# Performance work log

Hardware: AMD Instinct MI355X
Metric: run time of the kernel (lower is better)

The kernel has to match this reference:

```python
import jax, jax.numpy as jnp
import numpy as np

B, T, E, H = 4, 4096, 512, 64

def setup_inputs() -> dict:
    key = jax.random.key(0)
    k1, k2, k3, k4 = jax.random.split(key, 4)
    x = jax.random.normal(k1, (B, T, E), dtype=jnp.float32)
    # nn.Linear(E, H, bias=False) weight has shape [H, E]; y = x @ W.T
    Wq = jax.random.normal(k2, (H, E), dtype=jnp.float32) * (E ** -0.5)
    Wk = jax.random.normal(k3, (H, E), dtype=jnp.float32) * (E ** -0.5)
    Wv = jax.random.normal(k4, (H, E), dtype=jnp.float32) * (E ** -0.5)
    return {"x": x, "Wq": Wq, "Wk": Wk, "Wv": Wv}

def reference(x, Wq, Wk, Wv):
    # projections: [B, T, H]
    q = jnp.einsum('bte,he->bth', x, Wq)
    k = jnp.einsum('bte,he->bth', x, Wk)
    v = jnp.einsum('bte,he->bth', x, Wv)
    scale = 1.0 / jnp.sqrt(jnp.float32(q.shape[-1]))
    scores = jnp.einsum('bth,bsh->bts', q, k) * scale  # [B, T, T]
    t = scores.shape[-1]
    causal = jnp.tril(jnp.ones((t, t), dtype=bool))
    scores = jnp.where(causal, scores, -jnp.inf)
    probs = jax.nn.softmax(scores, axis=-1)
    # dropout p=0.0 (eval) -> identity
    return jnp.einsum('bts,bsh->bth', probs, v)
```

## Files before the change

kernel.cpp:

```cpp
#include <hip/hip_runtime.h>
#include <hip/hip_bf16.h>

#define Bn 4
#define Tn 4096
#define En 512
#define Hn 64
#define NEGINF -3e38f
#define QSCALE 0.1803368801f

typedef __attribute__((ext_vector_type(8))) __bf16 bf16x8;
typedef __attribute__((ext_vector_type(4))) __bf16 bf16x4;
typedef __attribute__((ext_vector_type(4))) float f32x4;

#define MFMA16(a, b, c) __builtin_amdgcn_mfma_f32_16x16x32_bf16(a, b, c, 0, 0, 0)

__device__ __forceinline__ unsigned short f2bf(float f) {
    union { float f; unsigned u; } v; v.f = f;
    unsigned r = v.u + 0x7fffu + ((v.u >> 16) & 1u);
    return (unsigned short)(r >> 16);
}
__device__ __forceinline__ float bf2f(unsigned short u) {
    union { unsigned u; float f; } v; v.u = ((unsigned)u) << 16;
    return v.f;
}
__device__ __forceinline__ unsigned cvtpk(float a, float b) {
    unsigned d;
    asm("v_cvt_pk_bf16_f32 %0, %1, %2" : "=v"(d) : "v"(a), "v"(b));
    return d;
}
__device__ __forceinline__ float exp2fast(float x) {
    float r;
    asm("v_exp_f32 %0, %1" : "=v"(r) : "v"(x));
    return r;
}
__device__ __forceinline__ void gl16(const void* g, void* l) {
    __builtin_amdgcn_global_load_lds(
        (const __attribute__((address_space(1))) unsigned int*)g,
        (__attribute__((address_space(3))) unsigned int*)l, 16, 0, 0);
}

__global__ void wcvt(const float* __restrict__ Wq, const float* __restrict__ Wk,
                     const float* __restrict__ Wv, unsigned short* __restrict__ Wo) {
    int i = blockIdx.x * 256 + threadIdx.x;
    int mat = i >> 15;
    int off = i & 32767;
    const float* s = (mat == 0) ? Wq : ((mat == 1) ? Wk : Wv);
    Wo[i] = f2bf(s[off]);
}

__launch_bounds__(256, 2)
__global__ void proj(const float* __restrict__ x, const unsigned short* __restrict__ Wo,
                     unsigned short* __restrict__ q16, unsigned short* __restrict__ k16,
                     unsigned short* __restrict__ vt16) {
    __shared__ __align__(16) unsigned char plds[2][28672];
    const int tid = threadIdx.x;
    const int w = tid >> 6, lane = tid & 63, r = lane & 15, g = lane >> 4;
    const int row0 = blockIdx.x * 32;
    const int rsel = (w & 1) * 16, csel = (w >> 1) * 96;

    const int srow = tid >> 3, skc = (tid & 7) * 8;
    const int sby = (tid & 7) * 16;

    f32x4 acc[6];
#pragma unroll
    for (int i = 0; i < 6; ++i) acc[i] = (f32x4){0.f, 0.f, 0.f, 0.f};

    {
        const float4* xp = (const float4*)&x[(row0 + srow) * En + skc];
        float4 f0 = xp[0], f1 = xp[1];
        union { bf16x8 v; unsigned u32[4]; } t;
        t.u32[0] = cvtpk(f0.x, f0.y); t.u32[1] = cvtpk(f0.z, f0.w);
        t.u32[2] = cvtpk(f1.x, f1.y); t.u32[3] = cvtpk(f1.z, f1.w);
        *(bf16x8*)&plds[0][srow * 128 + (sby ^ ((srow & 7) << 4))] = t.v;
#pragma unroll
        for (int c2 = 0; c2 < 6; ++c2) {
            int wrow = c2 * 32 + srow;
            bf16x8 wv = *(const bf16x8*)&Wo[wrow * En + skc];
            *(bf16x8*)&plds[0][4096 + wrow * 128 + (sby ^ ((wrow & 7) << 4))] = wv;
        }
    }
    __syncthreads();

    for (int s = 0; s < 8; ++s) {
        const int pp = s & 1;
        const bool more = (s < 7);
        float4 nf0, nf1;
        bf16x8 nw[6];
        if (more) {
            int k1 = (s + 1) * 64;
            const float4* xp = (const float4*)&x[(row0 + srow) * En + k1 + skc];
            nf0 = xp[0]; nf1 = xp[1];
#pragma unroll
            for (int c2 = 0; c2 < 6; ++c2) {
                int wrow = c2 * 32 + srow;
                nw[c2] = *(const bf16x8*)&Wo[wrow * En + k1 + skc];
            }
        }
        {
            const unsigned char* A = &plds[pp][0];
            const unsigned char* W = &plds[pp][4096];
            int arow = rsel + r, asw = (arow & 7) << 4;
            bf16x8 a0 = *(const bf16x8*)&A[arow * 128 + ((g * 16) ^ asw)];
            bf16x8 a1 = *(const bf16x8*)&A[arow * 128 + ((64 + g * 16) ^ asw)];
#pragma unroll
            for (int ct = 0; ct < 6; ++ct) {
                int wrow = csel + ct * 16 + r, wsw = (wrow & 7) << 4;
                bf16x8 b0 = *(const bf16x8*)&W[wrow * 128 + ((g * 16) ^ wsw)];
                bf16x8 b1 = *(const bf16x8*)&W[wrow * 128 + ((64 + g * 16) ^ wsw)];
                acc[ct] = MFMA16(a0, b0, acc[ct]);
                acc[ct] = MFMA16(a1, b1, acc[ct]);
            }
        }
        if (more) {
            unsigned char* D = &plds[pp ^ 1][0];
            union { bf16x8 v; unsigned u32[4]; } t;
            t.u32[0] = cvtpk(nf0.x, nf0.y); t.u32[1] = cvtpk(nf0.z, nf0.w);
            t.u32[2] = cvtpk(nf1.x, nf1.y); t.u32[3] = cvtpk(nf1.z, nf1.w);
            *(bf16x8*)&D[srow * 128 + (sby ^ ((srow & 7) << 4))] = t.v;
#pragma unroll
            for (int c2 = 0; c2 < 6; ++c2) {
                int wrow = c2 * 32 + srow;
                *(bf16x8*)&D[4096 + wrow * 128 + (sby ^ ((wrow & 7) << 4))] = nw[c2];
            }
        }
        __syncthreads();
    }
#pragma unroll
    for (int ct = 0; ct < 6; ++ct) {
        int n = csel + ct * 16 + r;
#pragma unroll
        for (int reg = 0; reg < 4; ++reg) {
            int gr = row0 + rsel + g * 4 + reg;
            if (n < 64) {
                q16[gr * 64 + n] = f2bf(acc[ct][reg] * QSCALE);
            } else if (n < 128) {
                k16[gr * 64 + (n - 64)] = f2bf(acc[ct][reg]);
            } else {
                int h = n - 128; int bb = gr >> 12; int t = gr & 4095;
                vt16[((bb * 64 + h) << 12) + t] = f2bf(acc[ct][reg]);
            }
        }
    }
}

__launch_bounds__(256, 4)
__global__ void attnp(const unsigned short* __restrict__ q16, const unsigned short* __restrict__ k16,
                      const unsigned short* __restrict__ vt16,
                      unsigned short* __restrict__ po, float* __restrict__ lp) {
    __shared__ __align__(16) unsigned char lds[2][16384];

    const int tid = threadIdx.x;
    const int w = tid >> 6, lane = tid & 63, r = lane & 15, g = lane >> 4;
    const int bid = blockIdx.x;
    const int k_ = bid >> 8, idx = bid & 255;
    const int s5 = idx >> 3, b = (idx >> 1) & 3, q1 = idx & 1;
    const int jt = (k_ & 1) ? s5 : 63 - s5;
    const int quarter = ((k_ >> 1) << 1) | q1;
    const size_t kbase = (size_t)b * Tn;
    const int q0 = jt * 64;
    const int nt = jt + 1;
    const int t0 = (quarter * nt) >> 2;
    const int tEnd = ((quarter + 1) * nt) >> 2;
    const int wq0 = q0 + w * 16;

    const unsigned short* Kb = k16 + kbase * 64;
    const unsigned short* Vb = vt16 + ((size_t)(b * 64) << 12);

    const int srl = lane >> 3, scb = (lane & 7) * 16;

    bf16x8 bq0, bq1;
    {
        const unsigned short* qp = &q16[(kbase + wq0 + r) * 64 + g * 8];
        bq0 = *(const bf16x8*)qp;
        bq1 = *(const bf16x8*)(qp + 32);
    }

    f32x4 o[4];
#pragma unroll
    for (int i = 0; i < 4; ++i) o[i] = (f32x4){0.f, 0.f, 0.f, 0.f};
    float l_ = 0.f;

    if (tEnd > t0) {
        int kv0 = t0 * 64;
#pragma unroll
        for (int i = 0; i < 4; ++i) {
            int cc = w * 4 + i;
            if (cc < 8) {
                int row = cc * 8 + srl, sw = (row & 7) << 4;
                gl16((const char*)Kb + (size_t)(kv0 + row) * 128 + (scb ^ sw),
                     &lds[0][cc * 1024]);
            } else {
                int h = (cc - 8) * 8 + srl, sw = (h & 7) << 4;
                gl16((const char*)Vb + (size_t)h * 8192 + (size_t)kv0 * 2 + (scb ^ sw),
                     &lds[0][cc * 1024]);
            }
        }
    }
    __syncthreads();

    int pp = 0;
    for (int it = t0; it < tEnd; ++it, pp ^= 1) {
        const bool more = (it + 1 < tEnd);
        if (more) {
            int nkv = (it + 1) * 64;
#pragma unroll
            for (int i = 0; i < 4; ++i) {
                int cc = w * 4 + i;
                if (cc < 8) {
                    int row = cc * 8 + srl, sw = (row & 7) << 4;
                    gl16((const char*)Kb + (size_t)(nkv + row) * 128 + (scb ^ sw),
                         &lds[pp ^ 1][cc * 1024]);
                } else {
                    int h = (cc - 8) * 8 + srl, sw = (h & 7) << 4;
                    gl16((const char*)Vb + (size_t)h * 8192 + (size_t)nkv * 2 + (scb ^ sw),
                         &lds[pp ^ 1][cc * 1024]);
                }
            }
        }
        const int kv0 = it * 64;
        if (kv0 <= wq0 + 15) {
            const unsigned char* K = &lds[pp][0];
            const unsigned char* V = &lds[pp][8192];
            f32x4 s4[4];
            __builtin_amdgcn_s_setprio(1);
#pragma unroll
            for (int ct = 0; ct < 4; ++ct) {
                int row = ct * 16 + r;
                int base = row * 128, sw = (row & 7) << 4;
                bf16x8 ak0 = *(const bf16x8*)&K[base + ((g * 16) ^ sw)];
                bf16x8 ak1 = *(const bf16x8*)&K[base + ((64 + g * 16) ^ sw)];
                f32x4 t = (f32x4){0.f, 0.f, 0.f, 0.f};
                t = MFMA16(ak0, bq0, t);
                t = MFMA16(ak1, bq1, t);
                s4[ct] = t;
            }
            __builtin_amdgcn_s_setprio(0);
            if (kv0 + 63 > wq0) {
                int qq = wq0 + r;
#pragma unroll
                for (int ct = 0; ct < 4; ++ct)
#pragma unroll
                    for (int reg = 0; reg < 4; ++reg) {
                        int kv = kv0 + ct * 16 + g * 4 + reg;
                        if (kv > qq) s4[ct][reg] = NEGINF;
                    }
            }
#pragma unroll
            for (int ct = 0; ct < 4; ++ct)
#pragma unroll
                for (int reg = 0; reg < 4; ++reg)
                    s4[ct][reg] = exp2fast(s4[ct][reg]);
            l_ += ((s4[0][0] + s4[0][1]) + (s4[0][2] + s4[0][3])) +
                  ((s4[1][0] + s4[1][1]) + (s4[1][2] + s4[1][3])) +
                  ((s4[2][0] + s4[2][1]) + (s4[2][2] + s4[2][3])) +
                  ((s4[3][0] + s4[3][1]) + (s4[3][2] + s4[3][3]));
            union { bf16x8 v; unsigned u32[4]; } pk[2];
#pragma unroll
            for (int kf = 0; kf < 2; ++kf) {
                pk[kf].u32[0] = cvtpk(s4[kf * 2][0], s4[kf * 2][1]);
                pk[kf].u32[1] = cvtpk(s4[kf * 2][2], s4[kf * 2][3]);
                pk[kf].u32[2] = cvtpk(s4[kf * 2 + 1][0], s4[kf * 2 + 1][1]);
                pk[kf].u32[3] = cvtpk(s4[kf * 2 + 1][2], s4[kf * 2 + 1][3]);
            }
            __builtin_amdgcn_s_setprio(1);
#pragma unroll
            for (int cth = 0; cth < 4; ++cth) {
                int h = cth * 16 + r;
                int vb = h * 128, sw2 = (h & 7) << 4;
#pragma unroll
                for (int kf = 0; kf < 2; ++kf) {
                    int off = kf * 64 + g * 8;
                    union { bf16x8 v; bf16x4 h4[2]; } vv;
                    vv.h4[0] = *(const bf16x4*)&V[vb + (off ^ sw2)];
                    vv.h4[1] = *(const bf16x4*)&V[vb + ((off + 32) ^ sw2)];
                    o[cth] = MFMA16(pk[kf].v, vv.v, o[cth]);
                }
            }
            __builtin_amdgcn_s_setprio(0);
        }
        __syncthreads();
    }

    const size_t qb = (size_t)quarter * 16384 + b * 4096;
#pragma unroll
    for (int cth = 0; cth < 4; ++cth)
#pragma unroll
        for (int reg = 0; reg < 4; ++reg)
            po[(qb + wq0 + g * 4 + reg) * 64 + cth * 16 + r] = f2bf(o[cth][reg]);
    lp[(qb + wq0 + r) * 4 + g] = l_;
}

__global__ void merge(const unsigned short* __restrict__ po, const float* __restrict__ lp,
                      float* __restrict__ out) {
    int t = blockIdx.x * 256 + threadIdx.x;
    int q = t >> 3, c8 = (t & 7) * 8;
    float L = 0.f;
#pragma unroll
    for (int c = 0; c < 4; ++c)
#pragma unroll
        for (int gg = 0; gg < 4; ++gg)
            L += lp[((size_t)c * 16384 + q) * 4 + gg];
    float inv = 1.0f / L;
    float acc[8] = {0.f, 0.f, 0.f, 0.f, 0.f, 0.f, 0.f, 0.f};
#pragma unroll
    for (int c = 0; c < 4; ++c) {
        union { uint4 v; unsigned short u[8]; } ld;
        ld.v = *(const uint4*)&po[((size_t)c * 16384 + q) * 64 + c8];
#pragma unroll
        for (int j = 0; j < 8; ++j) acc[j] += bf2f(ld.u[j]);
    }
    float4* op = (float4*)&out[(size_t)q * 64 + c8];
    op[0] = (float4){acc[0] * inv, acc[1] * inv, acc[2] * inv, acc[3] * inv};
    op[1] = (float4){acc[4] * inv, acc[5] * inv, acc[6] * inv, acc[7] * inv};
}

extern "C" void kernel_launch(void* const* d_in, const int* in_sizes, int n_in,
                              void* d_out, int out_size, void* d_ws, size_t ws_size,
                              hipStream_t stream) {
    const float* x  = (const float*)d_in[0];
    const float* Wq = (const float*)d_in[1];
    const float* Wk = (const float*)d_in[2];
    const float* Wv = (const float*)d_in[3];
    float* out = (float*)d_out;
    char* ws = (char*)d_ws;

    unsigned short* Wo  = (unsigned short*)ws;
    unsigned short* q16 = (unsigned short*)(ws + 196608);
    unsigned short* k16 = (unsigned short*)(ws + 2293760);
    unsigned short* v16 = (unsigned short*)(ws + 4390912);
    unsigned short* po  = (unsigned short*)(ws + 6488064);
    float*          lp  = (float*)(ws + 14876672);

    hipLaunchKernelGGL(wcvt, dim3(384), dim3(256), 0, stream, Wq, Wk, Wv, Wo);
    hipLaunchKernelGGL(proj, dim3(512), dim3(256), 0, stream, x, Wo, q16, k16, v16);
    hipLaunchKernelGGL(attnp, dim3(1024), dim3(256), 0, stream, q16, k16, v16, po, lp);
    hipLaunchKernelGGL(merge, dim3(512), dim3(256), 0, stream, po, lp, out);
}
```

Before: 45.24 us.

## Fuse weight conversion into projection and rebalance causal attention split-K pieces

Removes the separate weight-conversion kernel: the projection kernel now loads fp32 weights and converts them to bf16 in registers before staging them in LDS. Attention work is repartitioned so the long (late) query tiles are split into 6 KV pieces and the short ones into 4, for 1280 blocks instead of 1024. The merge kernel sums a variable number of partials to match, and the attention launch bound is raised to 5 blocks per CU. This trades one launch and one bf16 weight round-trip for doubled weight-load bytes per projection block and more register pressure in the attention kernel.

```diff
diff --git a/kernel.cpp b/kernel.cpp
--- a/kernel.cpp
+++ b/kernel.cpp
@@ -14,20 +14,20 @@
 
 #define MFMA16(a, b, c) __builtin_amdgcn_mfma_f32_16x16x32_bf16(a, b, c, 0, 0, 0)
 
+__device__ __forceinline__ float bf2f(unsigned short u) {
+    union { unsigned u; float f; } v; v.u = ((unsigned)u) << 16;
+    return v.f;
+}
+__device__ __forceinline__ unsigned cvtpk(float a, float b) {
+    unsigned d;
+    asm("v_cvt_pk_bf16_f32 %0, %1, %2" : "=v"(d) : "v"(a), "v"(b));
+    return d;
+}
 __device__ __forceinline__ unsigned short f2bf(float f) {
     union { float f; unsigned u; } v; v.f = f;
     unsigned r = v.u + 0x7fffu + ((v.u >> 16) & 1u);
     return (unsigned short)(r >> 16);
 }
-__device__ __forceinline__ float bf2f(unsigned short u) {
-    union { unsigned u; float f; } v; v.u = ((unsigned)u) << 16;
-    return v.f;
-}
-__device__ __forceinline__ unsigned cvtpk(float a, float b) {
-    unsigned d;
-    asm("v_cvt_pk_bf16_f32 %0, %1, %2" : "=v"(d) : "v"(a), "v"(b));
-    return d;
-}
 __device__ __forceinline__ float exp2fast(float x) {
     float r;
     asm("v_exp_f32 %0, %1" : "=v"(r) : "v"(x));
@@ -39,17 +39,9 @@
         (__attribute__((address_space(3))) unsigned int*)l, 16, 0, 0);
 }
 
-__global__ void wcvt(const float* __restrict__ Wq, const float* __restrict__ Wk,
-                     const float* __restrict__ Wv, unsigned short* __restrict__ Wo) {
-    int i = blockIdx.x * 256 + threadIdx.x;
-    int mat = i >> 15;
-    int off = i & 32767;
-    const float* s = (mat == 0) ? Wq : ((mat == 1) ? Wk : Wv);
-    Wo[i] = f2bf(s[off]);
-}
-
 __launch_bounds__(256, 2)
-__global__ void proj(const float* __restrict__ x, const unsigned short* __restrict__ Wo,
+__global__ void proj(const float* __restrict__ x, const float* __restrict__ Wq,
+                     const float* __restrict__ Wk, const float* __restrict__ Wv,
                      unsigned short* __restrict__ q16, unsigned short* __restrict__ k16,
                      unsigned short* __restrict__ vt16) {
     __shared__ __align__(16) unsigned char plds[2][28672];
@@ -74,9 +66,15 @@
         *(bf16x8*)&plds[0][srow * 128 + (sby ^ ((srow & 7) << 4))] = t.v;
 #pragma unroll
         for (int c2 = 0; c2 < 6; ++c2) {
+            const float* Ws = (c2 < 2) ? Wq : ((c2 < 4) ? Wk : Wv);
+            int wr = (c2 & 1) * 32 + srow;
+            const float4* wp = (const float4*)&Ws[wr * En + skc];
+            float4 w0 = wp[0], w1 = wp[1];
+            union { bf16x8 v; unsigned u32[4]; } tw;
+            tw.u32[0] = cvtpk(w0.x, w0.y); tw.u32[1] = cvtpk(w0.z, w0.w);
+            tw.u32[2] = cvtpk(w1.x, w1.y); tw.u32[3] = cvtpk(w1.z, w1.w);
             int wrow = c2 * 32 + srow;
-            bf16x8 wv = *(const bf16x8*)&Wo[wrow * En + skc];
-            *(bf16x8*)&plds[0][4096 + wrow * 128 + (sby ^ ((wrow & 7) << 4))] = wv;
+            *(bf16x8*)&plds[0][4096 + wrow * 128 + (sby ^ ((wrow & 7) << 4))] = tw.v;
         }
     }
     __syncthreads();
@@ -85,15 +83,17 @@
         const int pp = s & 1;
         const bool more = (s < 7);
         float4 nf0, nf1;
-        bf16x8 nw[6];
+        float4 nw0[6], nw1[6];
         if (more) {
             int k1 = (s + 1) * 64;
             const float4* xp = (const float4*)&x[(row0 + srow) * En + k1 + skc];
             nf0 = xp[0]; nf1 = xp[1];
 #pragma unroll
             for (int c2 = 0; c2 < 6; ++c2) {
-                int wrow = c2 * 32 + srow;
-                nw[c2] = *(const bf16x8*)&Wo[wrow * En + k1 + skc];
+                const float* Ws = (c2 < 2) ? Wq : ((c2 < 4) ? Wk : Wv);
+                int wr = (c2 & 1) * 32 + srow;
+                const float4* wp = (const float4*)&Ws[wr * En + k1 + skc];
+                nw0[c2] = wp[0]; nw1[c2] = wp[1];
             }
         }
         {
@@ -119,8 +119,11 @@
             *(bf16x8*)&D[srow * 128 + (sby ^ ((srow & 7) << 4))] = t.v;
 #pragma unroll
             for (int c2 = 0; c2 < 6; ++c2) {
+                union { bf16x8 v; unsigned u32[4]; } tw;
+                tw.u32[0] = cvtpk(nw0[c2].x, nw0[c2].y); tw.u32[1] = cvtpk(nw0[c2].z, nw0[c2].w);
+                tw.u32[2] = cvtpk(nw1[c2].x, nw1[c2].y); tw.u32[3] = cvtpk(nw1[c2].z, nw1[c2].w);
                 int wrow = c2 * 32 + srow;
-                *(bf16x8*)&D[4096 + wrow * 128 + (sby ^ ((wrow & 7) << 4))] = nw[c2];
+                *(bf16x8*)&D[4096 + wrow * 128 + (sby ^ ((wrow & 7) << 4))] = tw.v;
             }
         }
         __syncthreads();
@@ -143,7 +146,7 @@
     }
 }
 
-__launch_bounds__(256, 4)
+__launch_bounds__(256, 5)
 __global__ void attnp(const unsigned short* __restrict__ q16, const unsigned short* __restrict__ k16,
                       const unsigned short* __restrict__ vt16,
                       unsigned short* __restrict__ po, float* __restrict__ lp) {
@@ -152,15 +155,22 @@
     const int tid = threadIdx.x;
     const int w = tid >> 6, lane = tid & 63, r = lane & 15, g = lane >> 4;
     const int bid = blockIdx.x;
-    const int k_ = bid >> 8, idx = bid & 255;
+    const int page = bid >> 8, idx = bid & 255;
     const int s5 = idx >> 3, b = (idx >> 1) & 3, q1 = idx & 1;
-    const int jt = (k_ & 1) ? s5 : 63 - s5;
-    const int quarter = ((k_ >> 1) << 1) | q1;
+    int jt, piece, t0, tEnd;
+    if (page < 3) {
+        jt = 63 - s5;
+        int nt = jt + 1;
+        piece = page + 3 * q1;
+        t0 = (piece * nt) / 6; tEnd = ((piece + 1) * nt) / 6;
+    } else {
+        jt = s5;
+        int nt = jt + 1;
+        piece = (page - 3) + 2 * q1;
+        t0 = (piece * nt) / 4; tEnd = ((piece + 1) * nt) / 4;
+    }
     const size_t kbase = (size_t)b * Tn;
     const int q0 = jt * 64;
-    const int nt = jt + 1;
-    const int t0 = (quarter * nt) >> 2;
-    const int tEnd = ((quarter + 1) * nt) >> 2;
     const int wq0 = q0 + w * 16;
 
     const unsigned short* Kb = k16 + kbase * 64;
@@ -281,7 +291,7 @@
         __syncthreads();
     }
 
-    const size_t qb = (size_t)quarter * 16384 + b * 4096;
+    const size_t qb = (size_t)piece * 16384 + b * 4096;
 #pragma unroll
     for (int cth = 0; cth < 4; ++cth)
 #pragma unroll
@@ -294,16 +304,16 @@
                       float* __restrict__ out) {
     int t = blockIdx.x * 256 + threadIdx.x;
     int q = t >> 3, c8 = (t & 7) * 8;
+    int tloc = (q & 4095) >> 6;
+    int ns = (tloc >= 32) ? 6 : 4;
     float L = 0.f;
-#pragma unroll
-    for (int c = 0; c < 4; ++c)
+    for (int c = 0; c < ns; ++c)
 #pragma unroll
         for (int gg = 0; gg < 4; ++gg)
             L += lp[((size_t)c * 16384 + q) * 4 + gg];
     float inv = 1.0f / L;
     float acc[8] = {0.f, 0.f, 0.f, 0.f, 0.f, 0.f, 0.f, 0.f};
-#pragma unroll
-    for (int c = 0; c < 4; ++c) {
+    for (int c = 0; c < ns; ++c) {
         union { uint4 v; unsigned short u[8]; } ld;
         ld.v = *(const uint4*)&po[((size_t)c * 16384 + q) * 64 + c8];
 #pragma unroll
@@ -324,15 +334,13 @@
     float* out = (float*)d_out;
     char* ws = (char*)d_ws;
 
-    unsigned short* Wo  = (unsigned short*)ws;
-    unsigned short* q16 = (unsigned short*)(ws + 196608);
-    unsigned short* k16 = (unsigned short*)(ws + 2293760);
-    unsigned short* v16 = (unsigned short*)(ws + 4390912);
-    unsigned short* po  = (unsigned short*)(ws + 6488064);
-    float*          lp  = (float*)(ws + 14876672);
-
-    hipLaunchKernelGGL(wcvt, dim3(384), dim3(256), 0, stream, Wq, Wk, Wv, Wo);
-    hipLaunchKernelGGL(proj, dim3(512), dim3(256), 0, stream, x, Wo, q16, k16, v16);
-    hipLaunchKernelGGL(attnp, dim3(1024), dim3(256), 0, stream, q16, k16, v16, po, lp);
+    unsigned short* q16 = (unsigned short*)ws;
+    unsigned short* k16 = (unsigned short*)(ws + 2097152);
+    unsigned short* v16 = (unsigned short*)(ws + 4194304);
+    unsigned short* po  = (unsigned short*)(ws + 6291456);
+    float*          lp  = (float*)(ws + 18874368);
+
+    hipLaunchKernelGGL(proj, dim3(512), dim3(256), 0, stream, x, Wq, Wk, Wv, q16, k16, v16);
+    hipLaunchKernelGGL(attnp, dim3(1280), dim3(256), 0, stream, q16, k16, v16, po, lp);
     hipLaunchKernelGGL(merge, dim3(512), dim3(256), 0, stream, po, lp, out);
 }
```

Measured after the change: 46.76 us. 3.4% more time.
